# Performance work log

Measured on AMD Instinct MI355X. Metric: run time of the kernel, lower is better.

Reference implementation:

```python
import jax, jax.numpy as jnp
import numpy as np

DIM_Q = 512
DIM_K = 512
DIM_V = 512
NUM_HEADS = 8
B, NQ, NK = 8, 1024, 1024
EPS = 1e-5


def _layer_norm(x, gamma, beta):
    mu = jnp.mean(x, axis=-1, keepdims=True)
    var = jnp.var(x, axis=-1, keepdims=True)
    return (x - mu) * jax.lax.rsqrt(var + EPS) * gamma + beta


def setup_inputs() -> dict:
    key = jax.random.key(0)
    ks = jax.random.split(key, 12)

    def lin(k, fan_in, fan_out):
        bound = 1.0 / np.sqrt(fan_in)
        kw, kb = jax.random.split(k)
        W = jax.random.uniform(kw, (fan_in, fan_out), jnp.float32, -bound, bound)
        b = jax.random.uniform(kb, (fan_out,), jnp.float32, -bound, bound)
        return W, b

    Q = jax.random.normal(ks[0], (B, NQ, DIM_Q), jnp.float32)
    K = jax.random.normal(ks[1], (B, NK, DIM_K), jnp.float32)
    Wq, bq = lin(ks[2], DIM_Q, DIM_V)
    Wk, bk = lin(ks[3], DIM_K, DIM_V)
    Wv, bv = lin(ks[4], DIM_K, DIM_V)
    Wo, bo = lin(ks[5], DIM_V, DIM_V)
    g0 = jnp.ones((DIM_V,), jnp.float32)
    be0 = jnp.zeros((DIM_V,), jnp.float32)
    g1 = jnp.ones((DIM_V,), jnp.float32)
    be1 = jnp.zeros((DIM_V,), jnp.float32)
    return {"Q": Q, "K": K, "Wq": Wq, "bq": bq, "Wk": Wk, "bk": bk,
            "Wv": Wv, "bv": bv, "Wo": Wo, "bo": bo,
            "g0": g0, "be0": be0, "g1": g1, "be1": be1}


def reference(Q, K, Wq, bq, Wk, bk, Wv, bv, Wo, bo, g0, be0, g1, be1):
    H = NUM_HEADS
    d = DIM_V // H
    b, nq, _ = Q.shape
    nk = K.shape[1]

    Qp = (Q @ Wq + bq).reshape(b, nq, H, d)   # [B,Nq,H,d]
    Kp = (K @ Wk + bk).reshape(b, nk, H, d)   # [B,Nk,H,d]
    Vp = (K @ Wv + bv).reshape(b, nk, H, d)   # [B,Nk,H,d]

    # NOTE: original scales by sqrt(dim_V), not sqrt(head_dim)
    scores = jnp.einsum("bqhd,bkhd->bhqk", Qp, Kp) / jnp.sqrt(
        jnp.asarray(DIM_V, Qp.dtype))
    A = jax.nn.softmax(scores, axis=-1)                     # [B,H,Nq,Nk]
    O = Qp + jnp.einsum("bhqk,bkhd->bqhd", A, Vp)           # residual inside heads
    O = O.reshape(b, nq, DIM_V)
    O = _layer_norm(O, g0, be0)
    O = O + jax.nn.relu(O @ Wo + bo)
    O = _layer_norm(O, g1, be1)
    return O
```

## Files before the change

### kernel.cpp

```cpp
#include <hip/hip_runtime.h>
#include <hip/hip_bf16.h>

typedef __attribute__((ext_vector_type(8))) short short8;
typedef __attribute__((ext_vector_type(4))) short s16x4;
typedef __attribute__((ext_vector_type(4))) float f32x4;

#define DIMV 512
#define NHEAD 8
#define NBATCH 8
#define NQL 1024
#define NKL 1024
#define QSCALE (0.04419417382415922f * 1.44269504088896340f)

__device__ __forceinline__ short f2bf(float f) {
    unsigned int u = __float_as_uint(f);
    unsigned int r = (u + 0x7fffu + ((u >> 16) & 1u)) >> 16;
    return (short)r;
}
__device__ __forceinline__ float bf2f(short s) {
    return __uint_as_float(((unsigned int)(unsigned short)s) << 16);
}
__device__ __forceinline__ unsigned cvt_pk_bf16(float a, float b) {
    unsigned r;
    asm("v_cvt_pk_bf16_f32 %0, %1, %2" : "=v"(r) : "v"(a), "v"(b));
    return r;
}
__device__ __forceinline__ void gload16(const void* g, void* l) {
    __builtin_amdgcn_global_load_lds(
        (const __attribute__((address_space(1))) unsigned int*)g,
        (__attribute__((address_space(3))) unsigned int*)l, 16, 0, 0);
}

__global__ void k_cvt2(const float* __restrict__ a, const float* __restrict__ b,
                       short* __restrict__ oa, short* __restrict__ ob, int n) {
    const float* src = blockIdx.y ? b : a;
    short* dst = blockIdx.y ? ob : oa;
    int i = (blockIdx.x * blockDim.x + threadIdx.x) * 4;
    if (i < n) {
        float4 v = *reinterpret_cast<const float4*>(src + i);
        s16x4 o;
        o[0] = f2bf(v.x); o[1] = f2bf(v.y); o[2] = f2bf(v.z); o[3] = f2bf(v.w);
        *reinterpret_cast<s16x4*>(dst + i) = o;
    }
}

__global__ void k_transpose_w4(const float* __restrict__ w0, const float* __restrict__ w1,
                               const float* __restrict__ w2, const float* __restrict__ w3,
                               short* __restrict__ t0, short* __restrict__ t1,
                               short* __restrict__ t2, short* __restrict__ t3) {
    __shared__ float tile[32][33];
    const float* W; short* Wt;
    int z = blockIdx.z;
    if (z == 0)      { W = w0; Wt = t0; }
    else if (z == 1) { W = w1; Wt = t1; }
    else if (z == 2) { W = w2; Wt = t2; }
    else             { W = w3; Wt = t3; }
    int tx = threadIdx.x, ty = threadIdx.y;
    int n0 = blockIdx.x * 32, k0 = blockIdx.y * 32;
    #pragma unroll
    for (int r = 0; r < 4; ++r)
        tile[ty + r * 8][tx] = W[(size_t)(k0 + ty + r * 8) * DIMV + n0 + tx];
    __syncthreads();
    #pragma unroll
    for (int r = 0; r < 4; ++r)
        Wt[(size_t)(n0 + ty + r * 8) * DIMV + k0 + tx] = f2bf(tile[tx][ty + r * 8]);
}

__global__ __launch_bounds__(512) void k_gemm_qkv(
    const short* __restrict__ Qb, const short* __restrict__ Kb,
    const short* __restrict__ Wqt, const short* __restrict__ Wkvt,
    const float* __restrict__ bq, const float* __restrict__ bk,
    const float* __restrict__ bv,
    short* __restrict__ Qpb, short* __restrict__ Kp, short* __restrict__ VT)
{
    __shared__ __align__(16) short As[2][128 * 64];
    __shared__ __align__(16) short Bs[2][128 * 64];
    int tid = threadIdx.x;
    int lane = tid & 63, wv = tid >> 6;
    int wr = wv >> 2, wc = wv & 3;
    int c = lane & 15, g = lane >> 4;
    int bid = blockIdx.x;
    bool isQ = bid < 256;
    int lb = isQ ? bid : bid - 256;
    int NBX = isQ ? 4 : 8;
    int xcd = lb & 7, slot = lb >> 3;
    int bx = slot % NBX, by = xcd + 8 * (slot / NBX);
    int m0 = by * 128, n0 = bx * 128;
    const short* Ab = isQ ? Qb : Kb;
    const short* Bt = isQ ? Wqt : Wkvt;

    int lr = lane >> 3, ls = lane & 7;
    int sg = ls ^ lr;
    const short* Asrc = Ab + (size_t)(m0 + wv * 16 + lr) * 512 + sg * 8;
    const short* Bsrc = Bt + (size_t)(n0 + wv * 16 + lr) * 512 + sg * 8;

    #define STAGE_QKV(buf, k0)  do {                                          \
        _Pragma("unroll")                                                     \
        for (int L = 0; L < 2; ++L)                                           \
            gload16(Asrc + (k0) + L * 8 * 512, (char*)&As[buf][(wv*16+L*8)*64]);\
        _Pragma("unroll")                                                     \
        for (int L = 0; L < 2; ++L)                                           \
            gload16(Bsrc + (k0) + L * 8 * 512, (char*)&Bs[buf][(wv*16+L*8)*64]);\
    } while (0)

    STAGE_QKV(0, 0);
    __syncthreads();

    f32x4 acc[4][2] = {};
    for (int t = 0; t < 8; ++t) {
        int cur = t & 1;
        if (t < 7) STAGE_QKV(cur ^ 1, (t + 1) * 64);
        #pragma unroll
        for (int ks = 0; ks < 2; ++ks) {
            int sl = ((ks * 4 + g) ^ (c & 7)) * 8;
            short8 af[4], bf[2];
            #pragma unroll
            for (int i = 0; i < 4; ++i)
                af[i] = *reinterpret_cast<short8*>(&As[cur][(wr * 64 + i * 16 + c) * 64 + sl]);
            #pragma unroll
            for (int j = 0; j < 2; ++j)
                bf[j] = *reinterpret_cast<short8*>(&Bs[cur][(wc * 32 + j * 16 + c) * 64 + sl]);
            #pragma unroll
            for (int i = 0; i < 4; ++i)
                #pragma unroll
                for (int j = 0; j < 2; ++j)
                    acc[i][j] = __builtin_amdgcn_mfma_f32_16x16x32_bf16(af[i], bf[j], acc[i][j], 0, 0, 0);
        }
        __syncthreads();
    }

    int vb = m0 >> 10, kvb = m0 & 1023;
    #pragma unroll
    for (int i = 0; i < 4; ++i)
        #pragma unroll
        for (int j = 0; j < 2; ++j) {
            int rrow = wr * 64 + i * 16 + g * 4;
            int row = m0 + rrow;
            int col = n0 + wc * 32 + j * 16 + c;
            if (isQ) {
                float bb = bq[col];
                #pragma unroll
                for (int q = 0; q < 4; ++q)
                    Qpb[(size_t)(row + q) * 512 + col] = f2bf((acc[i][j][q] + bb) * QSCALE);
            } else if (col < 512) {
                float bb = bk[col];
                #pragma unroll
                for (int q = 0; q < 4; ++q)
                    Kp[(size_t)(row + q) * 512 + col] = f2bf(acc[i][j][q] + bb);
            } else {
                int colv = col - 512;
                float bb = bv[colv];
                s16x4 pk;
                #pragma unroll
                for (int q = 0; q < 4; ++q) pk[q] = f2bf(acc[i][j][q] + bb);
                *reinterpret_cast<s16x4*>(
                    &VT[((size_t)(vb * 512 + colv)) * 1024 + kvb + rrow]) = pk;
            }
        }
}

__global__ __launch_bounds__(256) void k_gemm_o(
    const short* __restrict__ A, const short* __restrict__ Bt,
    const float* __restrict__ bias, short* __restrict__ outB,
    const short* __restrict__ residB)
{
    __shared__ __align__(16) short As[2][128 * 64];
    __shared__ __align__(16) short Bs[2][64 * 64];
    int tid = threadIdx.x;
    int lane = tid & 63, wv = tid >> 6;
    int wr = wv >> 1, wc = wv & 1;
    int c = lane & 15, g = lane >> 4;
    int lb = blockIdx.x;
    int xcd = lb & 7, slot = lb >> 3;
    int bx = slot & 7, by = xcd + 8 * (slot >> 3);
    int m0 = by * 128, n0 = bx * 64;

    int lr = lane >> 3, ls = lane & 7;
    int sg = ls ^ lr;
    const short* Asrc = A + (size_t)(m0 + wv * 32 + lr) * 512 + sg * 8;
    const short* Bsrc = Bt + (size_t)(n0 + wv * 16 + lr) * 512 + sg * 8;

    #define STAGE_O(buf, k0)  do {                                            \
        _Pragma("unroll")                                                     \
        for (int L = 0; L < 4; ++L)                                           \
            gload16(Asrc + (k0) + L * 8 * 512, (char*)&As[buf][(wv*32+L*8)*64]);\
        _Pragma("unroll")                                                     \
        for (int L = 0; L < 2; ++L)                                           \
            gload16(Bsrc + (k0) + L * 8 * 512, (char*)&Bs[buf][(wv*16+L*8)*64]);\
    } while (0)

    STAGE_O(0, 0);
    __syncthreads();

    f32x4 acc[4][2] = {};
    for (int t = 0; t < 8; ++t) {
        int cur = t & 1;
        if (t < 7) STAGE_O(cur ^ 1, (t + 1) * 64);
        #pragma unroll
        for (int ks = 0; ks < 2; ++ks) {
            int sl = ((ks * 4 + g) ^ (c & 7)) * 8;
            short8 af[4], bf[2];
            #pragma unroll
            for (int i = 0; i < 4; ++i)
                af[i] = *reinterpret_cast<short8*>(&As[cur][(wr * 64 + i * 16 + c) * 64 + sl]);
            #pragma unroll
            for (int j = 0; j < 2; ++j)
                bf[j] = *reinterpret_cast<short8*>(&Bs[cur][(wc * 32 + j * 16 + c) * 64 + sl]);
            #pragma unroll
            for (int i = 0; i < 4; ++i)
                #pragma unroll
                for (int j = 0; j < 2; ++j)
                    acc[i][j] = __builtin_amdgcn_mfma_f32_16x16x32_bf16(af[i], bf[j], acc[i][j], 0, 0, 0);
        }
        __syncthreads();
    }

    #pragma unroll
    for (int i = 0; i < 4; ++i)
        #pragma unroll
        for (int j = 0; j < 2; ++j) {
            int row = m0 + wr * 64 + i * 16 + g * 4;
            int col = n0 + wc * 32 + j * 16 + c;
            float bb = bias[col];
            #pragma unroll
            for (int q = 0; q < 4; ++q) {
                size_t idx = (size_t)(row + q) * 512 + col;
                outB[idx] = f2bf(bf2f(residB[idx]) + fmaxf(acc[i][j][q] + bb, 0.f));
            }
        }
}

__global__ __launch_bounds__(512) void k_attn(
    const short* __restrict__ Qb, const short* __restrict__ Kb,
    const short* __restrict__ VTb, const short* __restrict__ RgBase,
    short* __restrict__ Out)
{
    constexpr float RSCALE = 1.0f / QSCALE;
    __shared__ __align__(16) short Ks[2][64 * 64];
    __shared__ __align__(16) short Vt[2][64 * 64];
    __shared__ __align__(16) short Ps[128 * 72];
    int tid = threadIdx.x;
    int lane = tid & 63, w = tid >> 6;
    int c = lane & 15, g = lane >> 4;
    int bid = blockIdx.x;
    int grp = bid & 63, qb = bid >> 6;
    int h = grp & 7, b = grp >> 3;
    const short* Qg = Qb + (size_t)(b * NQL + qb * 128) * 512 + h * 64;
    const short* Kg = Kb + (size_t)b * NKL * 512 + h * 64;
    const short* VTg = VTb + (size_t)(b * 512 + h * 64) * NKL;
    const short* Rg = RgBase + (size_t)(b * NQL + qb * 128) * 512 + h * 64;
    short* Og = Out + (size_t)(b * NQL + qb * 128) * 512 + h * 64;

    short8 qf[2];
    #pragma unroll
    for (int ks = 0; ks < 2; ++ks)
        qf[ks] = *reinterpret_cast<const short8*>(&Qg[(size_t)(w * 16 + c) * 512 + ks * 32 + g * 8]);

    int sr = tid >> 3, ss = tid & 7;
    int sg = ss ^ (sr & 7);
    const short* Kgc = Kg + (size_t)sr * 512 + sg * 8;
    const short* Vgc = VTg + (size_t)sr * 1024 + sg * 8;
    char* KsB = (char*)&Ks[0][0];
    char* VtB = (char*)&Vt[0][0];
    int wbase = (tid & ~63) * 16;

    gload16(Kgc, KsB + wbase);
    gload16(Vgc, VtB + wbase);
    __syncthreads();

    float m = -1e30f, l = 0.f;
    f32x4 o[4] = {};
    int swz = (c & 7) * 8;

    for (int t = 0; t < 16; ++t) {
        int cur = t & 1;
        if (t < 15) {
            int nxt = cur ^ 1;
            gload16(Kgc + (size_t)(t + 1) * 64 * 512, KsB + nxt * 8192 + wbase);
            gload16(Vgc + (t + 1) * 64, VtB + nxt * 8192 + wbase);
        }

        f32x4 s[4] = {};
        #pragma unroll
        for (int ks = 0; ks < 2; ++ks) {
            #pragma unroll
            for (int i = 0; i < 4; ++i) {
                short8 ak = *reinterpret_cast<short8*>(
                    &Ks[cur][(i * 16 + c) * 64 + (((ks * 4 + g) * 8) ^ swz)]);
                s[i] = __builtin_amdgcn_mfma_f32_16x16x32_bf16(ak, qf[ks], s[i], 0, 0, 0);
            }
        }

        float r0 = fmaxf(fmaxf(s[0][0], s[0][1]), fmaxf(s[0][2], s[0][3]));
        float r1 = fmaxf(fmaxf(s[1][0], s[1][1]), fmaxf(s[1][2], s[1][3]));
        float r2 = fmaxf(fmaxf(s[2][0], s[2][1]), fmaxf(s[2][2], s[2][3]));
        float r3 = fmaxf(fmaxf(s[3][0], s[3][1]), fmaxf(s[3][2], s[3][3]));
        float rowm = fmaxf(fmaxf(r0, r1), fmaxf(r2, r3));
        rowm = fmaxf(rowm, __shfl_xor(rowm, 16));
        rowm = fmaxf(rowm, __shfl_xor(rowm, 32));
        if (!__all(rowm <= m + 8.f)) {
            float mnew = fmaxf(m, rowm);
            float corr = __builtin_amdgcn_exp2f(m - mnew);
            l *= corr;
            float cq[4];
            #pragma unroll
            for (int q = 0; q < 4; ++q) cq[q] = __shfl(corr, g * 4 + q);
            #pragma unroll
            for (int jf = 0; jf < 4; ++jf)
                #pragma unroll
                for (int q = 0; q < 4; ++q)
                    o[jf][q] *= cq[q];
            m = mnew;
        }
        float psum = 0.f;
        #pragma unroll
        for (int i = 0; i < 4; ++i) {
            float p0 = __builtin_amdgcn_exp2f(s[i][0] - m);
            float p1 = __builtin_amdgcn_exp2f(s[i][1] - m);
            float p2 = __builtin_amdgcn_exp2f(s[i][2] - m);
            float p3 = __builtin_amdgcn_exp2f(s[i][3] - m);
            psum += (p0 + p1) + (p2 + p3);
            uint2 pw;
            pw.x = cvt_pk_bf16(p0, p1);
            pw.y = cvt_pk_bf16(p2, p3);
            *reinterpret_cast<uint2*>(&Ps[(w * 16 + c) * 72 + i * 16 + g * 4]) = pw;
        }
        psum += __shfl_xor(psum, 16);
        psum += __shfl_xor(psum, 32);
        l += psum;

        #pragma unroll
        for (int ks = 0; ks < 2; ++ks) {
            short8 pa = *reinterpret_cast<short8*>(&Ps[(w * 16 + c) * 72 + ks * 32 + g * 8]);
            #pragma unroll
            for (int jf = 0; jf < 4; ++jf) {
                short8 vb = *reinterpret_cast<short8*>(
                    &Vt[cur][(jf * 16 + c) * 64 + (((ks * 4 + g) * 8) ^ swz)]);
                o[jf] = __builtin_amdgcn_mfma_f32_16x16x32_bf16(pa, vb, o[jf], 0, 0, 0);
            }
        }

        __syncthreads();
    }

    float linv = 1.f / l;
    float lq[4];
    #pragma unroll
    for (int q = 0; q < 4; ++q) lq[q] = __shfl(linv, g * 4 + q);
    #pragma unroll
    for (int jf = 0; jf < 4; ++jf)
        #pragma unroll
        for (int q = 0; q < 4; ++q) {
            int r = w * 16 + g * 4 + q;
            int d = jf * 16 + c;
            size_t idx = (size_t)r * 512 + d;
            Og[idx] = f2bf(o[jf][q] * lq[q] + bf2f(Rg[idx]) * RSCALE);
        }
}

__global__ __launch_bounds__(64) void k_ln(
    const short* __restrict__ inB,
    float* __restrict__ outF, short* __restrict__ outB,
    const float* __restrict__ gamma, const float* __restrict__ beta)
{
    int row = blockIdx.x, lane = threadIdx.x;
    float vals[8];
    short8 v = *reinterpret_cast<const short8*>(&inB[(size_t)row * 512 + lane * 8]);
    #pragma unroll
    for (int j = 0; j < 8; ++j) vals[j] = bf2f(v[j]);
    float sum = 0.f, sq = 0.f;
    #pragma unroll
    for (int j = 0; j < 8; ++j) { sum += vals[j]; sq += vals[j] * vals[j]; }
    #pragma unroll
    for (int mask = 32; mask; mask >>= 1) {
        sum += __shfl_xor(sum, mask);
        sq  += __shfl_xor(sq, mask);
    }
    float mean = sum * (1.f / 512.f);
    float var  = sq * (1.f / 512.f) - mean * mean;
    float rstd = rsqrtf(var + 1e-5f);
    float y[8];
    #pragma unroll
    for (int j = 0; j < 8; ++j) {
        int col = lane * 8 + j;
        y[j] = (vals[j] - mean) * rstd * gamma[col] + beta[col];
    }
    size_t base = (size_t)row * 512 + lane * 8;
    if (outF) {
        float4 o0 = {y[0], y[1], y[2], y[3]};
        float4 o1 = {y[4], y[5], y[6], y[7]};
        *reinterpret_cast<float4*>(&outF[base]) = o0;
        *reinterpret_cast<float4*>(&outF[base + 4]) = o1;
    }
    if (outB) {
        int4 p;
        p.x = cvt_pk_bf16(y[0], y[1]); p.y = cvt_pk_bf16(y[2], y[3]);
        p.z = cvt_pk_bf16(y[4], y[5]); p.w = cvt_pk_bf16(y[6], y[7]);
        *reinterpret_cast<int4*>(&outB[base]) = p;
    }
}

extern "C" void kernel_launch(void* const* d_in, const int* in_sizes, int n_in,
                              void* d_out, int out_size, void* d_ws, size_t ws_size,
                              hipStream_t stream) {
    const float* Q   = (const float*)d_in[0];
    const float* K   = (const float*)d_in[1];
    const float* Wq  = (const float*)d_in[2];
    const float* bq  = (const float*)d_in[3];
    const float* Wk  = (const float*)d_in[4];
    const float* bk  = (const float*)d_in[5];
    const float* Wv  = (const float*)d_in[6];
    const float* bv  = (const float*)d_in[7];
    const float* Wo  = (const float*)d_in[8];
    const float* bo  = (const float*)d_in[9];
    const float* g0  = (const float*)d_in[10];
    const float* be0 = (const float*)d_in[11];
    const float* g1  = (const float*)d_in[12];
    const float* be1 = (const float*)d_in[13];
    float* out = (float*)d_out;
    char* ws = (char*)d_ws;
    const size_t MB = 1024 * 1024;

    short* Qb    = (short*)(ws + 0);
    short* Kb    = (short*)(ws + 8 * MB);
    short* Wqt   = (short*)(ws + 16 * MB);
    short* Wkvt  = (short*)(ws + 16 * MB + 512 * 1024);
    short* Wot   = (short*)(ws + 17 * MB + 512 * 1024);
    short* VT    = (short*)(ws + 18 * MB);
    short* Qpb   = (short*)(ws + 34 * MB);
    short* Kp    = (short*)(ws + 42 * MB);
    short* Oa    = (short*)(ws + 0);
    short* ln0b  = (short*)(ws + 34 * MB);
    short* out2b = (short*)(ws + 42 * MB);

    int n = NBATCH * NQL * DIMV;
    dim3 cg(n / 4 / 256, 2);
    k_cvt2<<<cg, 256, 0, stream>>>(Q, K, Qb, Kb, n);
    dim3 tb(32, 8), tg(16, 16, 4);
    k_transpose_w4<<<tg, tb, 0, stream>>>(Wq, Wk, Wv, Wo,
                                          Wqt, Wkvt, Wkvt + 512 * 512, Wot);

    k_gemm_qkv<<<768, 512, 0, stream>>>(Qb, Kb, Wqt, Wkvt, bq, bk, bv, Qpb, Kp, VT);

    k_attn<<<NBATCH * NHEAD * (NQL / 128), 512, 0, stream>>>(Qpb, Kp, VT, Qpb, Oa);

    k_ln<<<NBATCH * NQL, 64, 0, stream>>>(Oa, nullptr, ln0b, g0, be0);
    k_gemm_o<<<512, 256, 0, stream>>>(ln0b, Wot, bo, out2b, ln0b);
    k_ln<<<NBATCH * NQL, 64, 0, stream>>>(out2b, out, nullptr, g1, be1);
}
```

Measured before the change: 93.68 us.

## Give each attention wave two query tiles and merge preprocessing kernels

The attention kernel now runs with 4 waves instead of 8, and each wave handles 32 query rows as two 16-row tiles. Each K and V fragment read from LDS is reused for two MFMAs, which halves LDS traffic per FLOP, and the tile loads are split across fewer threads. The swizzle is rewritten into an equivalent index form. Separately, the bf16 conversion and weight transpose kernels are fused into one launch to save a launch. The trade-off is higher register pressure and fewer waves per block to hide latency.

```diff
diff --git a/kernel.cpp b/kernel.cpp
--- a/kernel.cpp
+++ b/kernel.cpp
@@ -31,39 +31,43 @@
         (__attribute__((address_space(3))) unsigned int*)l, 16, 0, 0);
 }
 
-__global__ void k_cvt2(const float* __restrict__ a, const float* __restrict__ b,
-                       short* __restrict__ oa, short* __restrict__ ob, int n) {
-    const float* src = blockIdx.y ? b : a;
-    short* dst = blockIdx.y ? ob : oa;
-    int i = (blockIdx.x * blockDim.x + threadIdx.x) * 4;
-    if (i < n) {
-        float4 v = *reinterpret_cast<const float4*>(src + i);
-        s16x4 o;
-        o[0] = f2bf(v.x); o[1] = f2bf(v.y); o[2] = f2bf(v.z); o[3] = f2bf(v.w);
-        *reinterpret_cast<s16x4*>(dst + i) = o;
-    }
-}
-
-__global__ void k_transpose_w4(const float* __restrict__ w0, const float* __restrict__ w1,
-                               const float* __restrict__ w2, const float* __restrict__ w3,
-                               short* __restrict__ t0, short* __restrict__ t1,
-                               short* __restrict__ t2, short* __restrict__ t3) {
+__global__ void k_pre(const float* __restrict__ Qf, const float* __restrict__ Kf,
+                      short* __restrict__ Qb, short* __restrict__ Kb,
+                      const float* __restrict__ w0, const float* __restrict__ w1,
+                      const float* __restrict__ w2, const float* __restrict__ w3,
+                      short* __restrict__ t0, short* __restrict__ t1,
+                      short* __restrict__ t2, short* __restrict__ t3, int n) {
     __shared__ float tile[32][33];
-    const float* W; short* Wt;
-    int z = blockIdx.z;
-    if (z == 0)      { W = w0; Wt = t0; }
-    else if (z == 1) { W = w1; Wt = t1; }
-    else if (z == 2) { W = w2; Wt = t2; }
-    else             { W = w3; Wt = t3; }
-    int tx = threadIdx.x, ty = threadIdx.y;
-    int n0 = blockIdx.x * 32, k0 = blockIdx.y * 32;
-    #pragma unroll
-    for (int r = 0; r < 4; ++r)
-        tile[ty + r * 8][tx] = W[(size_t)(k0 + ty + r * 8) * DIMV + n0 + tx];
-    __syncthreads();
-    #pragma unroll
-    for (int r = 0; r < 4; ++r)
-        Wt[(size_t)(n0 + ty + r * 8) * DIMV + k0 + tx] = f2bf(tile[tx][ty + r * 8]);
+    int tid = threadIdx.x;
+    if (blockIdx.y < 2) {
+        const float* src = blockIdx.y ? Kf : Qf;
+        short* dst = blockIdx.y ? Kb : Qb;
+        int i = (blockIdx.x * 256 + tid) * 4;
+        if (i < n) {
+            float4 v = *reinterpret_cast<const float4*>(src + i);
+            s16x4 o;
+            o[0] = f2bf(v.x); o[1] = f2bf(v.y); o[2] = f2bf(v.z); o[3] = f2bf(v.w);
+            *reinterpret_cast<s16x4*>(dst + i) = o;
+        }
+    } else {
+        int bid = blockIdx.x;
+        if (bid >= 1024) return;
+        int z = bid >> 8, t16 = bid & 255;
+        const float* W; short* Wt;
+        if (z == 0)      { W = w0; Wt = t0; }
+        else if (z == 1) { W = w1; Wt = t1; }
+        else if (z == 2) { W = w2; Wt = t2; }
+        else             { W = w3; Wt = t3; }
+        int tx = tid & 31, ty = tid >> 5;
+        int n0 = (t16 & 15) * 32, k0 = (t16 >> 4) * 32;
+        #pragma unroll
+        for (int r = 0; r < 4; ++r)
+            tile[ty + r * 8][tx] = W[(size_t)(k0 + ty + r * 8) * DIMV + n0 + tx];
+        __syncthreads();
+        #pragma unroll
+        for (int r = 0; r < 4; ++r)
+            Wt[(size_t)(n0 + ty + r * 8) * DIMV + k0 + tx] = f2bf(tile[tx][ty + r * 8]);
+    }
 }
 
 __global__ __launch_bounds__(512) void k_gemm_qkv(
@@ -230,7 +234,7 @@
         }
 }
 
-__global__ __launch_bounds__(512) void k_attn(
+__global__ __launch_bounds__(256) void k_attn(
     const short* __restrict__ Qb, const short* __restrict__ Kb,
     const short* __restrict__ VTb, const short* __restrict__ RgBase,
     short* __restrict__ Out)
@@ -240,7 +244,7 @@
     __shared__ __align__(16) short Vt[2][64 * 64];
     __shared__ __align__(16) short Ps[128 * 72];
     int tid = threadIdx.x;
-    int lane = tid & 63, w = tid >> 6;
+    int lane = tid & 63, wv = tid >> 6;
     int c = lane & 15, g = lane >> 4;
     int bid = blockIdx.x;
     int grp = bid & 63, qb = bid >> 6;
@@ -251,10 +255,13 @@
     const short* Rg = RgBase + (size_t)(b * NQL + qb * 128) * 512 + h * 64;
     short* Og = Out + (size_t)(b * NQL + qb * 128) * 512 + h * 64;
 
-    short8 qf[2];
-    #pragma unroll
-    for (int ks = 0; ks < 2; ++ks)
-        qf[ks] = *reinterpret_cast<const short8*>(&Qg[(size_t)(w * 16 + c) * 512 + ks * 32 + g * 8]);
+    short8 qf[2][2];
+    #pragma unroll
+    for (int jq = 0; jq < 2; ++jq)
+        #pragma unroll
+        for (int ks = 0; ks < 2; ++ks)
+            qf[jq][ks] = *reinterpret_cast<const short8*>(
+                &Qg[(size_t)(wv * 32 + jq * 16 + c) * 512 + ks * 32 + g * 8]);
 
     int sr = tid >> 3, ss = tid & 7;
     int sg = ss ^ (sr & 7);
@@ -265,97 +272,126 @@
     int wbase = (tid & ~63) * 16;
 
     gload16(Kgc, KsB + wbase);
+    gload16(Kgc + 32 * 512, KsB + 4096 + wbase);
     gload16(Vgc, VtB + wbase);
+    gload16(Vgc + 32 * 1024, VtB + 4096 + wbase);
     __syncthreads();
 
-    float m = -1e30f, l = 0.f;
-    f32x4 o[4] = {};
-    int swz = (c & 7) * 8;
+    float m[2] = {-1e30f, -1e30f}, l[2] = {0.f, 0.f};
+    f32x4 o[2][4] = {};
+    int swz = c & 7;
 
     for (int t = 0; t < 16; ++t) {
         int cur = t & 1;
         if (t < 15) {
-            int nxt = cur ^ 1;
-            gload16(Kgc + (size_t)(t + 1) * 64 * 512, KsB + nxt * 8192 + wbase);
-            gload16(Vgc + (t + 1) * 64, VtB + nxt * 8192 + wbase);
-        }
-
-        f32x4 s[4] = {};
+            int nb = (cur ^ 1) * 8192;
+            const short* Kn = Kgc + (size_t)(t + 1) * 64 * 512;
+            const short* Vn = Vgc + (t + 1) * 64;
+            gload16(Kn, KsB + nb + wbase);
+            gload16(Kn + 32 * 512, KsB + nb + 4096 + wbase);
+            gload16(Vn, VtB + nb + wbase);
+            gload16(Vn + 32 * 1024, VtB + nb + 4096 + wbase);
+        }
+
+        f32x4 s[4][2] = {};
         #pragma unroll
         for (int ks = 0; ks < 2; ++ks) {
             #pragma unroll
             for (int i = 0; i < 4; ++i) {
                 short8 ak = *reinterpret_cast<short8*>(
-                    &Ks[cur][(i * 16 + c) * 64 + (((ks * 4 + g) * 8) ^ swz)]);
-                s[i] = __builtin_amdgcn_mfma_f32_16x16x32_bf16(ak, qf[ks], s[i], 0, 0, 0);
-            }
-        }
-
-        float r0 = fmaxf(fmaxf(s[0][0], s[0][1]), fmaxf(s[0][2], s[0][3]));
-        float r1 = fmaxf(fmaxf(s[1][0], s[1][1]), fmaxf(s[1][2], s[1][3]));
-        float r2 = fmaxf(fmaxf(s[2][0], s[2][1]), fmaxf(s[2][2], s[2][3]));
-        float r3 = fmaxf(fmaxf(s[3][0], s[3][1]), fmaxf(s[3][2], s[3][3]));
-        float rowm = fmaxf(fmaxf(r0, r1), fmaxf(r2, r3));
-        rowm = fmaxf(rowm, __shfl_xor(rowm, 16));
-        rowm = fmaxf(rowm, __shfl_xor(rowm, 32));
-        if (!__all(rowm <= m + 8.f)) {
-            float mnew = fmaxf(m, rowm);
-            float corr = __builtin_amdgcn_exp2f(m - mnew);
-            l *= corr;
-            float cq[4];
-            #pragma unroll
-            for (int q = 0; q < 4; ++q) cq[q] = __shfl(corr, g * 4 + q);
-            #pragma unroll
-            for (int jf = 0; jf < 4; ++jf)
-                #pragma unroll
-                for (int q = 0; q < 4; ++q)
-                    o[jf][q] *= cq[q];
-            m = mnew;
-        }
-        float psum = 0.f;
-        #pragma unroll
-        for (int i = 0; i < 4; ++i) {
-            float p0 = __builtin_amdgcn_exp2f(s[i][0] - m);
-            float p1 = __builtin_amdgcn_exp2f(s[i][1] - m);
-            float p2 = __builtin_amdgcn_exp2f(s[i][2] - m);
-            float p3 = __builtin_amdgcn_exp2f(s[i][3] - m);
-            psum += (p0 + p1) + (p2 + p3);
-            uint2 pw;
-            pw.x = cvt_pk_bf16(p0, p1);
-            pw.y = cvt_pk_bf16(p2, p3);
-            *reinterpret_cast<uint2*>(&Ps[(w * 16 + c) * 72 + i * 16 + g * 4]) = pw;
-        }
-        psum += __shfl_xor(psum, 16);
-        psum += __shfl_xor(psum, 32);
-        l += psum;
+                    &Ks[cur][(i * 16 + c) * 64 + (((ks * 4 + g) ^ swz) * 8)]);
+                #pragma unroll
+                for (int jq = 0; jq < 2; ++jq)
+                    s[i][jq] = __builtin_amdgcn_mfma_f32_16x16x32_bf16(ak, qf[jq][ks], s[i][jq], 0, 0, 0);
+            }
+        }
+
+        float rowm[2];
+        #pragma unroll
+        for (int jq = 0; jq < 2; ++jq) {
+            float r0 = fmaxf(fmaxf(s[0][jq][0], s[0][jq][1]), fmaxf(s[0][jq][2], s[0][jq][3]));
+            float r1 = fmaxf(fmaxf(s[1][jq][0], s[1][jq][1]), fmaxf(s[1][jq][2], s[1][jq][3]));
+            float r2 = fmaxf(fmaxf(s[2][jq][0], s[2][jq][1]), fmaxf(s[2][jq][2], s[2][jq][3]));
+            float r3 = fmaxf(fmaxf(s[3][jq][0], s[3][jq][1]), fmaxf(s[3][jq][2], s[3][jq][3]));
+            float rm = fmaxf(fmaxf(r0, r1), fmaxf(r2, r3));
+            rm = fmaxf(rm, __shfl_xor(rm, 16));
+            rm = fmaxf(rm, __shfl_xor(rm, 32));
+            rowm[jq] = rm;
+        }
+        if (!__all((rowm[0] <= m[0] + 8.f) && (rowm[1] <= m[1] + 8.f))) {
+            #pragma unroll
+            for (int jq = 0; jq < 2; ++jq) {
+                float mnew = fmaxf(m[jq], rowm[jq]);
+                float corr = __builtin_amdgcn_exp2f(m[jq] - mnew);
+                l[jq] *= corr;
+                float cq[4];
+                #pragma unroll
+                for (int q = 0; q < 4; ++q) cq[q] = __shfl(corr, g * 4 + q);
+                #pragma unroll
+                for (int jf = 0; jf < 4; ++jf)
+                    #pragma unroll
+                    for (int q = 0; q < 4; ++q)
+                        o[jq][jf][q] *= cq[q];
+                m[jq] = mnew;
+            }
+        }
+        #pragma unroll
+        for (int jq = 0; jq < 2; ++jq) {
+            float psum = 0.f;
+            #pragma unroll
+            for (int i = 0; i < 4; ++i) {
+                float p0 = __builtin_amdgcn_exp2f(s[i][jq][0] - m[jq]);
+                float p1 = __builtin_amdgcn_exp2f(s[i][jq][1] - m[jq]);
+                float p2 = __builtin_amdgcn_exp2f(s[i][jq][2] - m[jq]);
+                float p3 = __builtin_amdgcn_exp2f(s[i][jq][3] - m[jq]);
+                psum += (p0 + p1) + (p2 + p3);
+                uint2 pw;
+                pw.x = cvt_pk_bf16(p0, p1);
+                pw.y = cvt_pk_bf16(p2, p3);
+                *reinterpret_cast<uint2*>(
+                    &Ps[(wv * 32 + jq * 16 + c) * 72 + i * 16 + g * 4]) = pw;
+            }
+            psum += __shfl_xor(psum, 16);
+            psum += __shfl_xor(psum, 32);
+            l[jq] += psum;
+        }
 
         #pragma unroll
         for (int ks = 0; ks < 2; ++ks) {
-            short8 pa = *reinterpret_cast<short8*>(&Ps[(w * 16 + c) * 72 + ks * 32 + g * 8]);
+            short8 pa[2];
+            #pragma unroll
+            for (int jq = 0; jq < 2; ++jq)
+                pa[jq] = *reinterpret_cast<short8*>(
+                    &Ps[(wv * 32 + jq * 16 + c) * 72 + ks * 32 + g * 8]);
             #pragma unroll
             for (int jf = 0; jf < 4; ++jf) {
                 short8 vb = *reinterpret_cast<short8*>(
-                    &Vt[cur][(jf * 16 + c) * 64 + (((ks * 4 + g) * 8) ^ swz)]);
-                o[jf] = __builtin_amdgcn_mfma_f32_16x16x32_bf16(pa, vb, o[jf], 0, 0, 0);
+                    &Vt[cur][(jf * 16 + c) * 64 + (((ks * 4 + g) ^ swz) * 8)]);
+                #pragma unroll
+                for (int jq = 0; jq < 2; ++jq)
+                    o[jq][jf] = __builtin_amdgcn_mfma_f32_16x16x32_bf16(pa[jq], vb, o[jq][jf], 0, 0, 0);
             }
         }
 
         __syncthreads();
     }
 
-    float linv = 1.f / l;
-    float lq[4];
-    #pragma unroll
-    for (int q = 0; q < 4; ++q) lq[q] = __shfl(linv, g * 4 + q);
-    #pragma unroll
-    for (int jf = 0; jf < 4; ++jf)
-        #pragma unroll
-        for (int q = 0; q < 4; ++q) {
-            int r = w * 16 + g * 4 + q;
-            int d = jf * 16 + c;
-            size_t idx = (size_t)r * 512 + d;
-            Og[idx] = f2bf(o[jf][q] * lq[q] + bf2f(Rg[idx]) * RSCALE);
-        }
+    #pragma unroll
+    for (int jq = 0; jq < 2; ++jq) {
+        float linv = 1.f / l[jq];
+        float lq[4];
+        #pragma unroll
+        for (int q = 0; q < 4; ++q) lq[q] = __shfl(linv, g * 4 + q);
+        #pragma unroll
+        for (int jf = 0; jf < 4; ++jf)
+            #pragma unroll
+            for (int q = 0; q < 4; ++q) {
+                int r = wv * 32 + jq * 16 + g * 4 + q;
+                int d = jf * 16 + c;
+                size_t idx = (size_t)r * 512 + d;
+                Og[idx] = f2bf(o[jq][jf][q] * lq[q] + bf2f(Rg[idx]) * RSCALE);
+            }
+    }
 }
 
 __global__ __launch_bounds__(64) void k_ln(
@@ -434,15 +470,13 @@
     short* out2b = (short*)(ws + 42 * MB);
 
     int n = NBATCH * NQL * DIMV;
-    dim3 cg(n / 4 / 256, 2);
-    k_cvt2<<<cg, 256, 0, stream>>>(Q, K, Qb, Kb, n);
-    dim3 tb(32, 8), tg(16, 16, 4);
-    k_transpose_w4<<<tg, tb, 0, stream>>>(Wq, Wk, Wv, Wo,
-                                          Wqt, Wkvt, Wkvt + 512 * 512, Wot);
+    dim3 pg(n / 4 / 256, 3);
+    k_pre<<<pg, 256, 0, stream>>>(Q, K, Qb, Kb, Wq, Wk, Wv, Wo,
+                                  Wqt, Wkvt, Wkvt + 512 * 512, Wot, n);
 
     k_gemm_qkv<<<768, 512, 0, stream>>>(Qb, Kb, Wqt, Wkvt, bq, bk, bv, Qpb, Kp, VT);
 
-    k_attn<<<NBATCH * NHEAD * (NQL / 128), 512, 0, stream>>>(Qpb, Kp, VT, Qpb, Oa);
+    k_attn<<<NBATCH * NHEAD * (NQL / 128), 256, 0, stream>>>(Qpb, Kp, VT, Qpb, Oa);
 
     k_ln<<<NBATCH * NQL, 64, 0, stream>>>(Oa, nullptr, ln0b, g0, be0);
     k_gemm_o<<<512, 256, 0, stream>>>(ln0b, Wot, bo, out2b, ln0b);
```

Result: slower. 96.93 us (+3.5%).
